# Kernel tuning notes

Hardware: AMD Instinct MI355X
Metric: run time of the kernel (lower is better)

## Reference

```python
import jax, jax.numpy as jnp
import numpy as np

DILATION = 6
KS = 3
N = KS * KS  # 9 kernel sample points
PAD = 1      # zero padding inside DeformConv2d
EPS = 1e-5


def conv2d(x, w, b=None, padding=0):
    out = jax.lax.conv_general_dilated(
        x, w, window_strides=(1, 1),
        padding=[(padding, padding), (padding, padding)],
        dimension_numbers=('NCHW', 'OIHW', 'NCHW'))
    if b is not None:
        out = out + b[None, :, None, None]
    return out


def batchnorm_train(x, gamma, beta):
    # training-mode BN (module default): batch statistics over (N,H,W)
    mean = x.mean(axis=(0, 2, 3), keepdims=True)
    var = x.var(axis=(0, 2, 3), keepdims=True)
    return gamma[None, :, None, None] * (x - mean) * jax.lax.rsqrt(var + EPS) + beta[None, :, None, None]


def deform_conv(x, p_w, p_b, m_w, m_b, d_w, d_b, w):
    b, c, h, wd = x.shape
    offset = conv2d(x, p_w, p_b, padding=1)                 # (b, 2N, h, w)
    m = jax.nn.sigmoid(conv2d(x, m_w, m_b, padding=1))      # (b, N, h, w) modulation
    s = 2.0 * jax.nn.sigmoid(conv2d(x, d_w, d_b, padding=1))  # (b,1,h,w) adaptive dilation scale (=1 at logit 0)
    xp = jnp.pad(x, ((0, 0), (0, 0), (PAD, PAD), (PAD, PAD)))
    Hp, Wp = h + 2 * PAD, wd + 2 * PAD
    # kernel grid p_n, row-major (kh, kw) to match conv weight layout
    rng = jnp.arange(-(KS - 1) // 2, (KS - 1) // 2 + 1, dtype=x.dtype)
    pn_x, pn_y = jnp.meshgrid(rng, rng, indexing='ij')
    pn_x, pn_y = pn_x.reshape(-1), pn_y.reshape(-1)          # (N,)
    # base sampling positions (offset by PAD into padded map)
    p0_x = jnp.arange(1, h + 1, dtype=x.dtype)[:, None, None]    # (h,1,1)
    p0_y = jnp.arange(1, wd + 1, dtype=x.dtype)[None, :, None]   # (1,w,1)
    off = offset.transpose(0, 2, 3, 1)   # (b,h,w,2N)
    s_ = s.transpose(0, 2, 3, 1)         # (b,h,w,1)
    px = p0_x + DILATION * s_ * pn_x + off[..., :N]   # (b,h,w,N)
    py = p0_y + DILATION * s_ * pn_y + off[..., N:]
    fx, fy = jnp.floor(px), jnp.floor(py)
    qx_lt = jnp.clip(fx, 0, Hp - 1).astype(jnp.int32)
    qy_lt = jnp.clip(fy, 0, Wp - 1).astype(jnp.int32)
    qx_rb = jnp.clip(fx + 1, 0, Hp - 1).astype(jnp.int32)
    qy_rb = jnp.clip(fy + 1, 0, Wp - 1).astype(jnp.int32)
    pxc = jnp.clip(px, 0, Hp - 1)
    pyc = jnp.clip(py, 0, Wp - 1)
    g_lt = (1 + (qx_lt - pxc)) * (1 + (qy_lt - pyc))
    g_rb = (1 - (qx_rb - pxc)) * (1 - (qy_rb - pyc))
    g_lb = (1 + (qx_lt - pxc)) * (1 - (qy_rb - pyc))
    g_rt = (1 - (qx_rb - pxc)) * (1 + (qy_lt - pyc))

    def gather(qx, qy):
        idx = (qx * Wp + qy).reshape(b, 1, -1)                    # (b,1,h*w*N)
        xf = xp.reshape(b, c, Hp * Wp)
        out = jnp.take_along_axis(xf, jnp.broadcast_to(idx, (b, c, idx.shape[-1])), axis=2)
        return out.reshape(b, c, h, wd, N)

    x_off = (g_lt[:, None] * gather(qx_lt, qy_lt)
             + g_rb[:, None] * gather(qx_rb, qy_rb)
             + g_lb[:, None] * gather(qx_lt, qy_rb)
             + g_rt[:, None] * gather(qx_rb, qy_lt))
    x_off = x_off * m.transpose(0, 2, 3, 1)[:, None]              # modulation
    # final 3x3 conv over gathered samples == contraction over (c, N)
    return jnp.einsum('bchwn,ocn->bohw', x_off, w.reshape(w.shape[0], c, N))


def setup_inputs() -> dict:
    key = jax.random.key(0)
    ks = jax.random.split(key, 12)
    cin, c1, c2 = 512, 256, 64
    b, h, w = 2, 96, 96
    def rn(k, shape, scale):
        return jax.random.normal(k, shape, dtype=jnp.float32) * scale
    return {
        'x': rn(ks[0], (b, cin, h, w), 1.0),
        'bn1_g': jnp.ones((cin,), jnp.float32),
        'bn1_b': jnp.zeros((cin,), jnp.float32),
        'conv1_w': rn(ks[1], (c1, cin, 1, 1), (1.0 / cin) ** 0.5),
        'conv1_b': jnp.zeros((c1,), jnp.float32),
        'bn2_g': jnp.ones((c1,), jnp.float32),
        'bn2_b': jnp.zeros((c1,), jnp.float32),
        'p_w': rn(ks[2], (2 * N, c1, 3, 3), 0.01),
        'p_b': jnp.zeros((2 * N,), jnp.float32),
        'm_w': rn(ks[3], (N, c1, 3, 3), 0.01),
        'm_b': jnp.zeros((N,), jnp.float32),
        'd_w': rn(ks[4], (1, c1, 3, 3), 0.01),
        'd_b': jnp.zeros((1,), jnp.float32),
        'dconv_w': rn(ks[5], (c2, c1, 3, 3), (1.0 / (c1 * 9)) ** 0.5),
    }


def reference(x, bn1_g, bn1_b, conv1_w, conv1_b, bn2_g, bn2_b,
              p_w, p_b, m_w, m_b, d_w, d_b, dconv_w):
    f = jax.nn.relu(batchnorm_train(x, bn1_g, bn1_b))
    f = conv2d(f, conv1_w, conv1_b)
    f = batchnorm_train(f, bn2_g, bn2_b)
    return deform_conv(f, p_w, p_b, m_w, m_b, d_w, d_b, dconv_w)
```

## Files before the change

### kernel.cpp

```cpp
#include <hip/hip_runtime.h>
#include <hip/hip_bf16.h>
#include <math.h>

#define BATCH 2
#define CIN 512
#define C1 256
#define C2 64
#define HH 96
#define WW 96
#define HWSZ 9216
#define NPIX 18432
#define HP 98
#define WP 98

typedef __attribute__((ext_vector_type(8))) short bf16x8;
typedef __attribute__((ext_vector_type(4))) short bf16x4;
typedef __attribute__((ext_vector_type(4))) float f32x4;
typedef __attribute__((ext_vector_type(4))) unsigned int u32x4;
typedef __attribute__((ext_vector_type(2))) unsigned int u32x2;
typedef unsigned short u16;
typedef unsigned int u32;

__device__ __forceinline__ float bfu2f(u16 u) {
  u32 v = ((u32)u) << 16; return __builtin_bit_cast(float, v);
}
__device__ __forceinline__ u16 f2bfu(float f) {
  return __builtin_bit_cast(u16, __float2bfloat16(f));
}
__device__ __forceinline__ float rd_any(const void* p, size_t i, int fl) {
  return fl ? bfu2f(((const u16*)p)[i]) : ((const float*)p)[i];
}
__device__ __forceinline__ int get_fl(const u32* g1raw) {
  return g1raw[0] != 0x3F800000u;
}
__device__ __forceinline__ bf16x8 lds_frag(const u16* p) {
  bf16x4 lo = *(const bf16x4*)p;
  bf16x4 hi = *(const bf16x4*)(p + 4);
  bf16x8 r;
  r[0] = lo[0]; r[1] = lo[1]; r[2] = lo[2]; r[3] = lo[3];
  r[4] = hi[0]; r[5] = hi[1]; r[6] = hi[2]; r[7] = hi[3];
  return r;
}
__device__ __forceinline__ void split4(const f32x4& v, u32x2& ph, u32x2& pl) {
  u16 h0 = f2bfu(v[0]), h1 = f2bfu(v[1]), h2 = f2bfu(v[2]), h3 = f2bfu(v[3]);
  u16 l0 = f2bfu(v[0] - bfu2f(h0)), l1 = f2bfu(v[1] - bfu2f(h1));
  u16 l2 = f2bfu(v[2] - bfu2f(h2)), l3 = f2bfu(v[3] - bfu2f(h3));
  ph = (u32x2){(u32)h0 | ((u32)h1 << 16), (u32)h2 | ((u32)h3 << 16)};
  pl = (u32x2){(u32)l0 | ((u32)l1 << 16), (u32)l2 | ((u32)l3 << 16)};
}

__global__ __launch_bounds__(256) void prep_kernel(
    const void* cw, const void* pw, const void* mw, const void* dw, const void* dcw,
    const void* cb, const void* g1, const void* b1, const void* g2, const void* b2,
    const void* pb, const void* mb, const void* db,
    u16* __restrict__ W1b, u16* __restrict__ W1l,
    u16* __restrict__ Wofa, u16* __restrict__ Wofal,
    u16* __restrict__ Wab, u16* __restrict__ Wabl,
    float* __restrict__ canon, float* __restrict__ statz) {
  int e = blockIdx.x * 256 + threadIdx.x;
  if (e >= 356380) return;
  int fl = get_fl((const u32*)g1);
  if (e < 131072) {
    float v = rd_any(cw, e, fl);
    u16 h = f2bfu(v);
    W1b[e] = h; W1l[e] = f2bfu(v - bfu2f(h));
  } else if (e < 204800) {
    int i = e - 131072;
    int tap = i >> 13; int r = i & 8191; int m = r >> 8; int c = r & 255;
    float v = 0.f;
    if (m < 18)       v = rd_any(pw, (size_t)(m * 256 + c) * 9 + tap, fl);
    else if (m < 27)  v = rd_any(mw, (size_t)((m - 18) * 256 + c) * 9 + tap, fl);
    else if (m == 27) v = rd_any(dw, (size_t)c * 9 + tap, fl);
    u16 h = f2bfu(v);
    Wofa[i] = h; Wofal[i] = f2bfu(v - bfu2f(h));
  } else if (e < 352256) {
    int i = e - 204800;
    int n = i >> 14; int r = i & 16383; int o = r >> 8; int c = r & 255;
    float v = rd_any(dcw, (size_t)(o * 256 + c) * 9 + n, fl);
    u16 h = f2bfu(v);
    Wab[i] = h; Wabl[i] = f2bfu(v - bfu2f(h));
  } else if (e < 354076) {
    int i = e - 352256;
    const void* src; int off;
    if      (i < 256)  { src = cb; off = i; }
    else if (i < 768)  { src = g1; off = i - 256; }
    else if (i < 1280) { src = b1; off = i - 768; }
    else if (i < 1536) { src = g2; off = i - 1280; }
    else if (i < 1792) { src = b2; off = i - 1536; }
    else if (i < 1810) { src = pb; off = i - 1792; }
    else if (i < 1819) { src = mb; off = i - 1810; }
    else               { src = db; off = i - 1819; }
    canon[i] = rd_any(src, off, fl);
  } else {
    statz[e - 354076] = 0.f;
  }
}

__global__ __launch_bounds__(256) void bn_stats_kernel(
    const void* __restrict__ x, const float* __restrict__ gamma,
    const float* __restrict__ beta, float* __restrict__ scale,
    float* __restrict__ shift, float* __restrict__ sums, float* __restrict__ sumsq,
    int* __restrict__ cnt, const u32* __restrict__ g1raw, int force, int C) {
  int c = blockIdx.x, part = blockIdx.y, tid = threadIdx.x;
  int fl = force ? 1 : get_fl(g1raw);
  int b = part >> 1, half = part & 1;
  size_t base = ((size_t)(b * C + c)) * HWSZ + half * (HWSZ / 2);
  float s = 0.f, q = 0.f;
  if (fl) {
    const u16* p = (const u16*)x + base;
    for (int i = tid; i < 576; i += 256) {
      u32x4 U = *(const u32x4*)(p + i * 8);
      #pragma unroll
      for (int k = 0; k < 4; ++k) {
        float v0 = bfu2f((u16)(U[k] & 0xffff));
        float v1 = bfu2f((u16)(U[k] >> 16));
        s += v0 + v1; q = fmaf(v0, v0, fmaf(v1, v1, q));
      }
    }
  } else {
    const float* p = (const float*)x + base;
    for (int i = tid; i < 1152; i += 256) {
      f32x4 v = *(const f32x4*)(p + i * 4);
      #pragma unroll
      for (int k = 0; k < 4; ++k) { s += v[k]; q = fmaf(v[k], v[k], q); }
    }
  }
  __shared__ float sh[512];
  sh[tid] = s; sh[tid + 256] = q;
  __syncthreads();
  for (int off = 128; off > 0; off >>= 1) {
    if (tid < off) { sh[tid] += sh[tid + off]; sh[tid + 256] += sh[tid + 256 + off]; }
    __syncthreads();
  }
  if (tid == 0) {
    atomicAdd(&sums[c], sh[0]);
    atomicAdd(&sumsq[c], sh[256]);
    __threadfence();
    int old = atomicAdd(&cnt[c], 1);
    if (old == 3) {
      float S = atomicAdd(&sums[c], 0.f);
      float Q = atomicAdd(&sumsq[c], 0.f);
      float mean = S * (1.f / (float)NPIX);
      float var  = fmaxf(Q * (1.f / (float)NPIX) - mean * mean, 0.f);
      float sc = gamma[c] * rsqrtf(var + 1e-5f);
      scale[c] = sc;
      shift[c] = beta[c] - mean * sc;
    }
  }
}

__global__ __launch_bounds__(256) void conv1x1_kernel(
    const void* __restrict__ x, const u16* __restrict__ W1b, const u16* __restrict__ W1l,
    const float* __restrict__ cb, const float* __restrict__ scale,
    const float* __restrict__ shift, const u32* __restrict__ g1raw,
    u16* __restrict__ f1) {
  __shared__ u16 Bh[64][68];
  __shared__ u16 Bl[64][68];
  int tid = threadIdx.x;
  int fl = get_fl(g1raw);
  int bxr = blockIdx.x;
  int bx = (bxr & 7) * 36 + (bxr >> 3);
  int p0 = bx * 64;
  int co0 = blockIdx.y * 128;
  int b = p0 / HWSZ;
  int hw0 = p0 % HWSZ;
  int lane = tid & 63, wv = tid >> 6, quad = lane >> 4, mr = lane & 15;
  int m0 = co0 + wv * 32;
  f32x4 acc[2][4];
  #pragma unroll
  for (int i = 0; i < 2; ++i)
    #pragma unroll
    for (int j = 0; j < 4; ++j) acc[i][j] = (f32x4){0.f, 0.f, 0.f, 0.f};

  int spx = tid & 63, cg = tid >> 6;
  int gpx = hw0 + spx;
  for (int c0 = 0; c0 < CIN; c0 += 64) {
    __syncthreads();
    #pragma unroll
    for (int j = 0; j < 8; ++j) {
      int ci = c0 + cg * 16 + j * 2;
      float v0, v1;
      if (fl) {
        const u16* xb = (const u16*)x;
        v0 = bfu2f(xb[((size_t)(b * CIN + ci)) * HWSZ + gpx]);
        v1 = bfu2f(xb[((size_t)(b * CIN + ci + 1)) * HWSZ + gpx]);
      } else {
        const float* xf = (const float*)x;
        v0 = xf[((size_t)(b * CIN + ci)) * HWSZ + gpx];
        v1 = xf[((size_t)(b * CIN + ci + 1)) * HWSZ + gpx];
      }
      v0 = fmaxf(fmaf(v0, scale[ci], shift[ci]), 0.f);
      v1 = fmaxf(fmaf(v1, scale[ci + 1], shift[ci + 1]), 0.f);
      u16 h0 = f2bfu(v0), h1 = f2bfu(v1);
      u16 l0 = f2bfu(v0 - bfu2f(h0)), l1 = f2bfu(v1 - bfu2f(h1));
      *(u32*)&Bh[spx][cg * 16 + j * 2] = (u32)h0 | ((u32)h1 << 16);
      *(u32*)&Bl[spx][cg * 16 + j * 2] = (u32)l0 | ((u32)l1 << 16);
    }
    __syncthreads();
    #pragma unroll
    for (int kk2 = 0; kk2 < 2; ++kk2) {
      int kk = kk2 * 32;
      #pragma unroll
      for (int mf = 0; mf < 2; ++mf) {
        size_t wix = (size_t)(m0 + mf * 16 + mr) * CIN + c0 + kk + quad * 8;
        bf16x8 ah = *(const bf16x8*)(W1b + wix);
        bf16x8 al = *(const bf16x8*)(W1l + wix);
        #pragma unroll
        for (int nt = 0; nt < 4; ++nt) {
          bf16x8 bl = lds_frag(&Bl[nt * 16 + mr][kk + quad * 8]);
          bf16x8 bh = lds_frag(&Bh[nt * 16 + mr][kk + quad * 8]);
          acc[mf][nt] = __builtin_amdgcn_mfma_f32_16x16x32_bf16(ah, bl, acc[mf][nt], 0, 0, 0);
          acc[mf][nt] = __builtin_amdgcn_mfma_f32_16x16x32_bf16(al, bh, acc[mf][nt], 0, 0, 0);
          acc[mf][nt] = __builtin_amdgcn_mfma_f32_16x16x32_bf16(ah, bh, acc[mf][nt], 0, 0, 0);
        }
      }
    }
  }
  #pragma unroll
  for (int mf = 0; mf < 2; ++mf) {
    #pragma unroll
    for (int nt = 0; nt < 4; ++nt) {
      #pragma unroll
      for (int r = 0; r < 4; ++r) {
        int co = m0 + mf * 16 + quad * 4 + r;
        f1[((size_t)(b * C1 + co)) * HWSZ + hw0 + nt * 16 + mr] = f2bfu(acc[mf][nt][r] + cb[co]);
      }
    }
  }
}

__global__ __launch_bounds__(256) void bn2pad_kernel(
    const u16* __restrict__ f1, const float* __restrict__ scale,
    const float* __restrict__ shift, float* __restrict__ xpf) {
  int bid = blockIdx.x;
  int ht = bid % 144; int ct = (bid / 144) & 3; int b = bid / 576;
  int hw0 = ht * 64, c0 = ct * 64;
  __shared__ float t[64][65];
  int tid = threadIdx.x;
  #pragma unroll
  for (int it = 0; it < 16; ++it) {
    int e = it * 256 + tid;
    int p = e & 63, ci = e >> 6;
    float v = bfu2f(f1[((size_t)(b * C1 + c0 + ci)) * HWSZ + hw0 + p]);
    t[ci][p] = fmaf(v, scale[c0 + ci], shift[c0 + ci]);
  }
  __syncthreads();
  #pragma unroll
  for (int it = 0; it < 16; ++it) {
    int e = it * 256 + tid;
    int ci = e & 63, p = e >> 6;
    int hw = hw0 + p; int h = hw / WW; int w = hw % WW;
    xpf[(((size_t)(b * HP) + h + 1) * WP + w + 1) * C1 + c0 + ci] = t[ci][p];
  }
}

__global__ __launch_bounds__(256) void init_kernel(
    const u32* __restrict__ g1raw, void* __restrict__ outv,
    float* __restrict__ oscr, float* __restrict__ opart, float* __restrict__ xpf) {
  int i = blockIdx.x * 256 + threadIdx.x;
  if (i < 1179648) {
    if (get_fl(g1raw)) { ((u16*)outv)[i] = 0; oscr[i] = 0.f; }
    else               { ((float*)outv)[i] = 0.f; }
  } else if (i < 1769472) {
    opart[i - 1179648] = 0.f;
  } else {
    int k = i - 1769472;
    int ch = k & 255; int pxi = k >> 8;
    int bb = pxi / 388; int r = pxi % 388;
    int h, w;
    if (r < 98)      { h = 0;  w = r; }
    else if (r < 196){ h = 97; w = r - 98; }
    else if (r < 292){ h = r - 196 + 1; w = 0; }
    else             { h = r - 292 + 1; w = 97; }
    xpf[(((size_t)(bb * HP) + h) * WP + w) * C1 + ch] = 0.f;
  }
}

__global__ __launch_bounds__(256) void offconv_kernel(
    const float* __restrict__ xpf, const u16* __restrict__ Wofa, const u16* __restrict__ Wofal,
    const float* __restrict__ pbc, const float* __restrict__ mbc,
    const float* __restrict__ dbc, float* __restrict__ opart) {
  __shared__ u16 Vh[32][68];
  __shared__ u16 Vl[32][68];
  int tid = threadIdx.x;
  int bxr = blockIdx.x;
  int bx = (bxr & 7) * 72 + (bxr >> 3);
  int tg = blockIdx.y;
  int p0 = bx * 32;
  int b = p0 / HWSZ;
  int hw = p0 % HWSZ; int h0 = hw / WW; int w0 = hw % WW;
  int lane = tid & 63, wv = tid >> 6, quad = lane >> 4, mr = lane & 15;
  int m0 = (wv & 1) * 16;
  int ntile = wv >> 1;
  int srow = tid >> 4;
  int scol = (tid & 15) * 4;
  f32x4 acc = (f32x4){0.f, 0.f, 0.f, 0.f};
  for (int tt = 0; tt < 3; ++tt) {
    int tap = tg * 3 + tt;
    int th = tap / 3, tw = tap % 3;
    const float* base = xpf + ((size_t)(b * HP + h0 + th) * WP + (w0 + tw)) * C1;
    for (int c0i = 0; c0i < 4; ++c0i) {
      int c0 = c0i * 64;
      if (tt | c0i) __syncthreads();
      #pragma unroll
      for (int pass = 0; pass < 2; ++pass) {
        int px = pass * 16 + srow;
        f32x4 v = *(const f32x4*)(base + (size_t)px * C1 + c0 + scol);
        u32x2 ph, pl;
        split4(v, ph, pl);
        *(u32x2*)&Vh[px][scol] = ph;
        *(u32x2*)&Vl[px][scol] = pl;
      }
      __syncthreads();
      #pragma unroll
      for (int kk2 = 0; kk2 < 2; ++kk2) {
        int kof = kk2 * 32 + quad * 8;
        size_t wix = (size_t)(tap * 32 + m0 + mr) * C1 + c0 + kof;
        bf16x8 ah = *(const bf16x8*)(Wofa + wix);
        bf16x8 al = *(const bf16x8*)(Wofal + wix);
        bf16x8 bl = lds_frag(&Vl[ntile * 16 + mr][kof]);
        bf16x8 bh = lds_frag(&Vh[ntile * 16 + mr][kof]);
        acc = __builtin_amdgcn_mfma_f32_16x16x32_bf16(ah, bl, acc, 0, 0, 0);
        acc = __builtin_amdgcn_mfma_f32_16x16x32_bf16(al, bh, acc, 0, 0, 0);
        acc = __builtin_amdgcn_mfma_f32_16x16x32_bf16(ah, bh, acc, 0, 0, 0);
      }
    }
  }
  int px = ntile * 16 + mr;
  #pragma unroll
  for (int r = 0; r < 4; ++r) {
    int m = m0 + quad * 4 + r;
    if (m < 28) {
      float v = acc[r];
      if (tg == 0) v += (m < 18) ? pbc[m] : ((m < 27) ? mbc[m - 18] : dbc[0]);
      atomicAdd(&opart[(size_t)m * NPIX + p0 + px], v);
    }
  }
}

__global__ __launch_bounds__(256) void deform_kernel(
    const float* __restrict__ xpf, const u16* __restrict__ Wab, const u16* __restrict__ Wabl,
    const float* __restrict__ opart, const u32* __restrict__ g1raw,
    float* __restrict__ oscr, void* __restrict__ outv) {
  __shared__ u16   Vh[64][68];
  __shared__ u16   Vl[64][68];
  __shared__ int   smi[4][64];
  __shared__ float smw[4][64];
  int tid = threadIdx.x;
  int bxr = blockIdx.x;
  int bx = (bxr & 7) * 36 + (bxr >> 3);
  int n = blockIdx.y;
  int p0 = bx * 64;
  int b = p0 / HWSZ;
  int hw0 = p0 % HWSZ;

  if (tid < 64) {
    int p = tid;
    int bp = p0 + p;
    int hw = hw0 + p; int h = hw / WW; int w = hw % WW;
    float offx = opart[(size_t)n * NPIX + bp];
    float offy = opart[(size_t)(9 + n) * NPIX + bp];
    float mlog = opart[(size_t)(18 + n) * NPIX + bp];
    float slog = opart[(size_t)27 * NPIX + bp];
    float mm = 1.f / (1.f + expf(-mlog));
    float s  = 2.f / (1.f + expf(-slog));
    float pnx = (float)(n / 3 - 1), pny = (float)(n % 3 - 1);
    float px = (float)(h + 1) + 6.f * s * pnx + offx;
    float py = (float)(w + 1) + 6.f * s * pny + offy;
    float fx = floorf(px), fy = floorf(py);
    float qxlt = fminf(fmaxf(fx, 0.f), 97.f);
    float qylt = fminf(fmaxf(fy, 0.f), 97.f);
    float qxrb = fminf(fmaxf(fx + 1.f, 0.f), 97.f);
    float qyrb = fminf(fmaxf(fy + 1.f, 0.f), 97.f);
    float pxc = fminf(fmaxf(px, 0.f), 97.f);
    float pyc = fminf(fmaxf(py, 0.f), 97.f);
    float glt = (1.f + (qxlt - pxc)) * (1.f + (qylt - pyc));
    float grb = (1.f - (qxrb - pxc)) * (1.f - (qyrb - pyc));
    float glb = (1.f + (qxlt - pxc)) * (1.f - (qyrb - pyc));
    float grt = (1.f - (qxrb - pxc)) * (1.f + (qylt - pyc));
    int ixlt = (int)qxlt, iylt = (int)qylt, ixrb = (int)qxrb, iyrb = (int)qyrb;
    int base = b * (HP * WP);
    smi[0][p] = base + ixlt * WP + iylt;  smw[0][p] = glt * mm;
    smi[1][p] = base + ixrb * WP + iyrb;  smw[1][p] = grb * mm;
    smi[2][p] = base + ixlt * WP + iyrb;  smw[2][p] = glb * mm;
    smi[3][p] = base + ixrb * WP + iylt;  smw[3][p] = grt * mm;
  }
  __syncthreads();

  int lane = tid & 63, wv = tid >> 6, quad = lane >> 4, mr = lane & 15;
  int m0 = wv * 16;
  int srow = tid >> 4;
  int scol = (tid & 15) * 4;
  f32x4 acc[4];
  #pragma unroll
  for (int i = 0; i < 4; ++i) acc[i] = (f32x4){0.f, 0.f, 0.f, 0.f};

  for (int c0i = 0; c0i < 4; ++c0i) {
    int c0 = c0i * 64;
    if (c0i) __syncthreads();
    #pragma unroll
    for (int pass = 0; pass < 4; ++pass) {
      int px = pass * 16 + srow;
      const float* r0 = xpf + (size_t)smi[0][px] * C1 + c0 + scol;
      const float* r1 = xpf + (size_t)smi[1][px] * C1 + c0 + scol;
      const float* r2 = xpf + (size_t)smi[2][px] * C1 + c0 + scol;
      const float* r3 = xpf + (size_t)smi[3][px] * C1 + c0 + scol;
      float w0 = smw[0][px], w1 = smw[1][px], w2 = smw[2][px], w3 = smw[3][px];
      f32x4 v0 = *(const f32x4*)r0;
      f32x4 v1 = *(const f32x4*)r1;
      f32x4 v2 = *(const f32x4*)r2;
      f32x4 v3 = *(const f32x4*)r3;
      f32x4 vc;
      #pragma unroll
      for (int j = 0; j < 4; ++j)
        vc[j] = fmaf(w0, v0[j], fmaf(w1, v1[j], fmaf(w2, v2[j], w3 * v3[j])));
      u32x2 ph, pl;
      split4(vc, ph, pl);
      *(u32x2*)&Vh[px][scol] = ph;
      *(u32x2*)&Vl[px][scol] = pl;
    }
    __syncthreads();
    #pragma unroll
    for (int kk2 = 0; kk2 < 2; ++kk2) {
      int kof = kk2 * 32 + quad * 8;
      size_t wix = (size_t)(n * C2 + m0 + mr) * C1 + c0 + kof;
      bf16x8 ah = *(const bf16x8*)(Wab + wix);
      bf16x8 al = *(const bf16x8*)(Wabl + wix);
      #pragma unroll
      for (int nt = 0; nt < 4; ++nt) {
        bf16x8 bl = lds_frag(&Vl[nt * 16 + mr][kof]);
        bf16x8 bh = lds_frag(&Vh[nt * 16 + mr][kof]);
        acc[nt] = __builtin_amdgcn_mfma_f32_16x16x32_bf16(ah, bl, acc[nt], 0, 0, 0);
        acc[nt] = __builtin_amdgcn_mfma_f32_16x16x32_bf16(al, bh, acc[nt], 0, 0, 0);
        acc[nt] = __builtin_amdgcn_mfma_f32_16x16x32_bf16(ah, bh, acc[nt], 0, 0, 0);
      }
    }
  }
  int fl = get_fl(g1raw);
  float* tgt = fl ? oscr : (float*)outv;
  #pragma unroll
  for (int nt = 0; nt < 4; ++nt) {
    #pragma unroll
    for (int r = 0; r < 4; ++r) {
      int o = m0 + quad * 4 + r;
      int hw = hw0 + nt * 16 + mr;
      atomicAdd(&tgt[((size_t)(b * C2 + o)) * HWSZ + hw], acc[nt][r]);
    }
  }
}

__global__ void cvt_out_kernel(const u32* __restrict__ g1raw,
                               const float* __restrict__ oscr, void* __restrict__ outv) {
  if (!get_fl(g1raw)) return;
  int i = blockIdx.x * 256 + threadIdx.x;
  ((u16*)outv)[i] = f2bfu(oscr[i]);
}

extern "C" void kernel_launch(void* const* d_in, const int* in_sizes, int n_in,
                              void* d_out, int out_size, void* d_ws, size_t ws_size,
                              hipStream_t stream) {
  const void* x       = d_in[0];
  const void* bn1_g   = d_in[1];
  const void* bn1_b   = d_in[2];
  const void* conv1_w = d_in[3];
  const void* conv1_b = d_in[4];
  const void* bn2_g   = d_in[5];
  const void* bn2_b   = d_in[6];
  const void* p_w     = d_in[7];
  const void* p_b     = d_in[8];
  const void* m_w     = d_in[9];
  const void* m_b     = d_in[10];
  const void* d_w     = d_in[11];
  const void* d_b     = d_in[12];
  const void* dconv_w = d_in[13];
  const u32* g1raw = (const u32*)bn1_g;

  float* ws = (float*)d_ws;
  float* canon = ws + 16;
  float* cbc = canon + 0;
  float* g1c = canon + 256;
  float* b1c = canon + 768;
  float* g2c = canon + 1280;
  float* b2c = canon + 1536;
  float* pbc = canon + 1792;
  float* mbc = canon + 1810;
  float* dbc = canon + 1819;
  float* scale1 = ws + 1840;
  float* shift1 = ws + 2352;
  float* scale2 = ws + 2864;
  float* shift2 = ws + 3120;
  float* statz  = ws + 3376;
  float* sums1  = statz;
  float* sumsq1 = statz + 512;
  int*   cnt1   = (int*)(statz + 1024);
  float* sums2  = statz + 1536;
  float* sumsq2 = statz + 1792;
  int*   cnt2   = (int*)(statz + 2048);
  u16* W1b   = (u16*)(ws + 5680);
  u16* W1l   = (u16*)(ws + 71216);
  u16* Wofa  = (u16*)(ws + 136752);
  u16* Wofal = (u16*)(ws + 173616);
  u16* Wab   = (u16*)(ws + 210480);
  u16* Wabl  = (u16*)(ws + 284208);
  u16* f1    = (u16*)(ws + 357936);
  float* oscr  = ws + 357936;
  float* opart = ws + 1537584;
  float* xpf   = ws + 2717232;

  prep_kernel<<<1393, 256, 0, stream>>>(conv1_w, p_w, m_w, d_w, dconv_w,
                                        conv1_b, bn1_g, bn1_b, bn2_g, bn2_b,
                                        p_b, m_b, d_b,
                                        W1b, W1l, Wofa, Wofal, Wab, Wabl, canon, statz);
  bn_stats_kernel<<<dim3(CIN, 4), 256, 0, stream>>>(x, g1c, b1c, scale1, shift1,
                                                    sums1, sumsq1, cnt1, g1raw, 0, CIN);
  conv1x1_kernel<<<dim3(288, 2), 256, 0, stream>>>(x, W1b, W1l, cbc, scale1, shift1, g1raw, f1);
  bn_stats_kernel<<<dim3(C1, 4), 256, 0, stream>>>(f1, g2c, b2c, scale2, shift2,
                                                   sums2, sumsq2, cnt2, g1raw, 1, C1);
  bn2pad_kernel<<<1152, 256, 0, stream>>>(f1, scale2, shift2, xpf);
  init_kernel<<<7688, 256, 0, stream>>>(g1raw, d_out, oscr, opart, xpf);
  offconv_kernel<<<dim3(576, 3), 256, 0, stream>>>(xpf, Wofa, Wofal, pbc, mbc, dbc, opart);
  deform_kernel<<<dim3(288, 9), 256, 0, stream>>>(xpf, Wab, Wabl, opart, g1raw, oscr, d_out);
  cvt_out_kernel<<<4608, 256, 0, stream>>>(g1raw, oscr, d_out);
}
```

Measured before the change: 321.5 us.

## Double-buffer LDS tiles and prefetch next K-chunk into registers in three GEMM kernels

```diff
diff --git a/kernel.cpp b/kernel.cpp
--- a/kernel.cpp
+++ b/kernel.cpp
@@ -154,8 +154,8 @@
     const float* __restrict__ cb, const float* __restrict__ scale,
     const float* __restrict__ shift, const u32* __restrict__ g1raw,
     u16* __restrict__ f1) {
-  __shared__ u16 Bh[64][68];
-  __shared__ u16 Bl[64][68];
+  __shared__ u16 Bh[2][64][68];
+  __shared__ u16 Bl[2][64][68];
   int tid = threadIdx.x;
   int fl = get_fl(g1raw);
   int bxr = blockIdx.x;
@@ -174,29 +174,43 @@
 
   int spx = tid & 63, cg = tid >> 6;
   int gpx = hw0 + spx;
-  for (int c0 = 0; c0 < CIN; c0 += 64) {
-    __syncthreads();
+
+  float pva[8], pvb[8];
+  auto ISSUE = [&](int c0) {
     #pragma unroll
     for (int j = 0; j < 8; ++j) {
       int ci = c0 + cg * 16 + j * 2;
-      float v0, v1;
       if (fl) {
         const u16* xb = (const u16*)x;
-        v0 = bfu2f(xb[((size_t)(b * CIN + ci)) * HWSZ + gpx]);
-        v1 = bfu2f(xb[((size_t)(b * CIN + ci + 1)) * HWSZ + gpx]);
+        pva[j] = bfu2f(xb[((size_t)(b * CIN + ci)) * HWSZ + gpx]);
+        pvb[j] = bfu2f(xb[((size_t)(b * CIN + ci + 1)) * HWSZ + gpx]);
       } else {
         const float* xf = (const float*)x;
-        v0 = xf[((size_t)(b * CIN + ci)) * HWSZ + gpx];
-        v1 = xf[((size_t)(b * CIN + ci + 1)) * HWSZ + gpx];
+        pva[j] = xf[((size_t)(b * CIN + ci)) * HWSZ + gpx];
+        pvb[j] = xf[((size_t)(b * CIN + ci + 1)) * HWSZ + gpx];
       }
-      v0 = fmaxf(fmaf(v0, scale[ci], shift[ci]), 0.f);
-      v1 = fmaxf(fmaf(v1, scale[ci + 1], shift[ci + 1]), 0.f);
+    }
+  };
+  auto COMBINE = [&](int buf, int c0) {
+    #pragma unroll
+    for (int j = 0; j < 8; ++j) {
+      int ci = c0 + cg * 16 + j * 2;
+      float v0 = fmaxf(fmaf(pva[j], scale[ci], shift[ci]), 0.f);
+      float v1 = fmaxf(fmaf(pvb[j], scale[ci + 1], shift[ci + 1]), 0.f);
       u16 h0 = f2bfu(v0), h1 = f2bfu(v1);
       u16 l0 = f2bfu(v0 - bfu2f(h0)), l1 = f2bfu(v1 - bfu2f(h1));
-      *(u32*)&Bh[spx][cg * 16 + j * 2] = (u32)h0 | ((u32)h1 << 16);
-      *(u32*)&Bl[spx][cg * 16 + j * 2] = (u32)l0 | ((u32)l1 << 16);
-    }
+      *(u32*)&Bh[buf][spx][cg * 16 + j * 2] = (u32)h0 | ((u32)h1 << 16);
+      *(u32*)&Bl[buf][spx][cg * 16 + j * 2] = (u32)l0 | ((u32)l1 << 16);
+    }
+  };
+
+  ISSUE(0);
+  COMBINE(0, 0);
+  for (int c8 = 0; c8 < 8; ++c8) {
     __syncthreads();
+    if (c8 < 7) ISSUE((c8 + 1) * 64);
+    int bsel = c8 & 1;
+    int c0 = c8 * 64;
     #pragma unroll
     for (int kk2 = 0; kk2 < 2; ++kk2) {
       int kk = kk2 * 32;
@@ -207,14 +221,15 @@
         bf16x8 al = *(const bf16x8*)(W1l + wix);
         #pragma unroll
         for (int nt = 0; nt < 4; ++nt) {
-          bf16x8 bl = lds_frag(&Bl[nt * 16 + mr][kk + quad * 8]);
-          bf16x8 bh = lds_frag(&Bh[nt * 16 + mr][kk + quad * 8]);
+          bf16x8 bl = lds_frag(&Bl[bsel][nt * 16 + mr][kk + quad * 8]);
+          bf16x8 bh = lds_frag(&Bh[bsel][nt * 16 + mr][kk + quad * 8]);
           acc[mf][nt] = __builtin_amdgcn_mfma_f32_16x16x32_bf16(ah, bl, acc[mf][nt], 0, 0, 0);
           acc[mf][nt] = __builtin_amdgcn_mfma_f32_16x16x32_bf16(al, bh, acc[mf][nt], 0, 0, 0);
           acc[mf][nt] = __builtin_amdgcn_mfma_f32_16x16x32_bf16(ah, bh, acc[mf][nt], 0, 0, 0);
         }
       }
     }
+    if (c8 < 7) COMBINE(bsel ^ 1, (c8 + 1) * 64);
   }
   #pragma unroll
   for (int mf = 0; mf < 2; ++mf) {
@@ -280,8 +295,8 @@
     const float* __restrict__ xpf, const u16* __restrict__ Wofa, const u16* __restrict__ Wofal,
     const float* __restrict__ pbc, const float* __restrict__ mbc,
     const float* __restrict__ dbc, float* __restrict__ opart) {
-  __shared__ u16 Vh[32][68];
-  __shared__ u16 Vl[32][68];
+  __shared__ u16 Vh[2][32][68];
+  __shared__ u16 Vl[2][32][68];
   int tid = threadIdx.x;
   int bxr = blockIdx.x;
   int bx = (bxr & 7) * 72 + (bxr >> 3);
@@ -295,36 +310,51 @@
   int srow = tid >> 4;
   int scol = (tid & 15) * 4;
   f32x4 acc = (f32x4){0.f, 0.f, 0.f, 0.f};
-  for (int tt = 0; tt < 3; ++tt) {
-    int tap = tg * 3 + tt;
+
+  f32x4 pv[2];
+  auto ISSUE = [&](int it) {
+    int tap = tg * 3 + (it >> 2);
     int th = tap / 3, tw = tap % 3;
+    int c0 = (it & 3) * 64;
     const float* base = xpf + ((size_t)(b * HP + h0 + th) * WP + (w0 + tw)) * C1;
-    for (int c0i = 0; c0i < 4; ++c0i) {
-      int c0 = c0i * 64;
-      if (tt | c0i) __syncthreads();
-      #pragma unroll
-      for (int pass = 0; pass < 2; ++pass) {
-        int px = pass * 16 + srow;
-        f32x4 v = *(const f32x4*)(base + (size_t)px * C1 + c0 + scol);
-        u32x2 ph, pl;
-        split4(v, ph, pl);
-        *(u32x2*)&Vh[px][scol] = ph;
-        *(u32x2*)&Vl[px][scol] = pl;
-      }
-      __syncthreads();
-      #pragma unroll
-      for (int kk2 = 0; kk2 < 2; ++kk2) {
-        int kof = kk2 * 32 + quad * 8;
-        size_t wix = (size_t)(tap * 32 + m0 + mr) * C1 + c0 + kof;
-        bf16x8 ah = *(const bf16x8*)(Wofa + wix);
-        bf16x8 al = *(const bf16x8*)(Wofal + wix);
-        bf16x8 bl = lds_frag(&Vl[ntile * 16 + mr][kof]);
-        bf16x8 bh = lds_frag(&Vh[ntile * 16 + mr][kof]);
-        acc = __builtin_amdgcn_mfma_f32_16x16x32_bf16(ah, bl, acc, 0, 0, 0);
-        acc = __builtin_amdgcn_mfma_f32_16x16x32_bf16(al, bh, acc, 0, 0, 0);
-        acc = __builtin_amdgcn_mfma_f32_16x16x32_bf16(ah, bh, acc, 0, 0, 0);
-      }
-    }
+    #pragma unroll
+    for (int pass = 0; pass < 2; ++pass) {
+      int px = pass * 16 + srow;
+      pv[pass] = *(const f32x4*)(base + (size_t)px * C1 + c0 + scol);
+    }
+  };
+  auto COMBINE = [&](int buf) {
+    #pragma unroll
+    for (int pass = 0; pass < 2; ++pass) {
+      int px = pass * 16 + srow;
+      u32x2 ph, pl;
+      split4(pv[pass], ph, pl);
+      *(u32x2*)&Vh[buf][px][scol] = ph;
+      *(u32x2*)&Vl[buf][px][scol] = pl;
+    }
+  };
+
+  ISSUE(0);
+  COMBINE(0);
+  for (int it = 0; it < 12; ++it) {
+    __syncthreads();
+    if (it < 11) ISSUE(it + 1);
+    int bsel = it & 1;
+    int tap = tg * 3 + (it >> 2);
+    int c0 = (it & 3) * 64;
+    #pragma unroll
+    for (int kk2 = 0; kk2 < 2; ++kk2) {
+      int kof = kk2 * 32 + quad * 8;
+      size_t wix = (size_t)(tap * 32 + m0 + mr) * C1 + c0 + kof;
+      bf16x8 ah = *(const bf16x8*)(Wofa + wix);
+      bf16x8 al = *(const bf16x8*)(Wofal + wix);
+      bf16x8 bl = lds_frag(&Vl[bsel][ntile * 16 + mr][kof]);
+      bf16x8 bh = lds_frag(&Vh[bsel][ntile * 16 + mr][kof]);
+      acc = __builtin_amdgcn_mfma_f32_16x16x32_bf16(ah, bl, acc, 0, 0, 0);
+      acc = __builtin_amdgcn_mfma_f32_16x16x32_bf16(al, bh, acc, 0, 0, 0);
+      acc = __builtin_amdgcn_mfma_f32_16x16x32_bf16(ah, bh, acc, 0, 0, 0);
+    }
+    if (it < 11) COMBINE(bsel ^ 1);
   }
   int px = ntile * 16 + mr;
   #pragma unroll
@@ -342,8 +372,8 @@
     const float* __restrict__ xpf, const u16* __restrict__ Wab, const u16* __restrict__ Wabl,
     const float* __restrict__ opart, const u32* __restrict__ g1raw,
     float* __restrict__ oscr, void* __restrict__ outv) {
-  __shared__ u16   Vh[64][68];
-  __shared__ u16   Vl[64][68];
+  __shared__ u16   Vh[2][64][68];
+  __shared__ u16   Vl[2][64][68];
   __shared__ int   smi[4][64];
   __shared__ float smw[4][64];
   int tid = threadIdx.x;
@@ -395,31 +425,41 @@
   #pragma unroll
   for (int i = 0; i < 4; ++i) acc[i] = (f32x4){0.f, 0.f, 0.f, 0.f};
 
-  for (int c0i = 0; c0i < 4; ++c0i) {
-    int c0 = c0i * 64;
-    if (c0i) __syncthreads();
+  f32x4 pv[4][4];
+  auto ISSUE = [&](int c0) {
     #pragma unroll
     for (int pass = 0; pass < 4; ++pass) {
       int px = pass * 16 + srow;
-      const float* r0 = xpf + (size_t)smi[0][px] * C1 + c0 + scol;
-      const float* r1 = xpf + (size_t)smi[1][px] * C1 + c0 + scol;
-      const float* r2 = xpf + (size_t)smi[2][px] * C1 + c0 + scol;
-      const float* r3 = xpf + (size_t)smi[3][px] * C1 + c0 + scol;
+      #pragma unroll
+      for (int k = 0; k < 4; ++k)
+        pv[pass][k] = *(const f32x4*)(xpf + (size_t)smi[k][px] * C1 + c0 + scol);
+    }
+  };
+  auto COMBINE = [&](int buf) {
+    #pragma unroll
+    for (int pass = 0; pass < 4; ++pass) {
+      int px = pass * 16 + srow;
       float w0 = smw[0][px], w1 = smw[1][px], w2 = smw[2][px], w3 = smw[3][px];
-      f32x4 v0 = *(const f32x4*)r0;
-      f32x4 v1 = *(const f32x4*)r1;
-      f32x4 v2 = *(const f32x4*)r2;
-      f32x4 v3 = *(const f32x4*)r3;
       f32x4 vc;
       #pragma unroll
       for (int j = 0; j < 4; ++j)
-        vc[j] = fmaf(w0, v0[j], fmaf(w1, v1[j], fmaf(w2, v2[j], w3 * v3[j])));
+        vc[j] = fmaf(w0, pv[pass][0][j],
+                fmaf(w1, pv[pass][1][j],
+                fmaf(w2, pv[pass][2][j], w3 * pv[pass][3][j])));
       u32x2 ph, pl;
       split4(vc, ph, pl);
-      *(u32x2*)&Vh[px][scol] = ph;
-      *(u32x2*)&Vl[px][scol] = pl;
-    }
+      *(u32x2*)&Vh[buf][px][scol] = ph;
+      *(u32x2*)&Vl[buf][px][scol] = pl;
+    }
+  };
+
+  ISSUE(0);
+  COMBINE(0);
+  for (int c0i = 0; c0i < 4; ++c0i) {
     __syncthreads();
+    if (c0i < 3) ISSUE((c0i + 1) * 64);
+    int bsel = c0i & 1;
+    int c0 = c0i * 64;
     #pragma unroll
     for (int kk2 = 0; kk2 < 2; ++kk2) {
       int kof = kk2 * 32 + quad * 8;
@@ -428,13 +468,14 @@
       bf16x8 al = *(const bf16x8*)(Wabl + wix);
       #pragma unroll
       for (int nt = 0; nt < 4; ++nt) {
-        bf16x8 bl = lds_frag(&Vl[nt * 16 + mr][kof]);
-        bf16x8 bh = lds_frag(&Vh[nt * 16 + mr][kof]);
+        bf16x8 bl = lds_frag(&Vl[bsel][nt * 16 + mr][kof]);
+        bf16x8 bh = lds_frag(&Vh[bsel][nt * 16 + mr][kof]);
         acc[nt] = __builtin_amdgcn_mfma_f32_16x16x32_bf16(ah, bl, acc[nt], 0, 0, 0);
         acc[nt] = __builtin_amdgcn_mfma_f32_16x16x32_bf16(al, bh, acc[nt], 0, 0, 0);
         acc[nt] = __builtin_amdgcn_mfma_f32_16x16x32_bf16(ah, bh, acc[nt], 0, 0, 0);
       }
     }
+    if (c0i < 3) COMBINE(bsel ^ 1);
   }
   int fl = get_fl(g1raw);
   float* tgt = fl ? oscr : (float*)outv;
```

Result: faster. 308.4 us (-4.1%).
